# Kernel tuning notes

Hardware: AMD Instinct MI355X
Metric: run time of the kernel (lower is better)

The kernel has to match this reference:

```python
import jax, jax.numpy as jnp
import numpy as np

B, T, SD, AD, H, K, HID = 256, 128, 8, 2, 3, 4, 256


def setup_inputs() -> dict:
    key = jax.random.key(0)
    ks = jax.random.split(key, 12)
    inp = {
        "state": jax.random.normal(ks[0], (B, T, SD), dtype=jnp.float32),
        "action": jax.random.normal(ks[1], (B, T, AD), dtype=jnp.float32),
        # Linear(4, 4*H, bias=False): weight (4*H, 4)
        "Wk": jax.random.normal(ks[2], (4 * H, K), dtype=jnp.float32) * 0.1,
        "Wq": jax.random.normal(ks[3], (4 * H, SD + AD), dtype=jnp.float32) * 0.1,
        "Wv": jax.random.normal(ks[4], (4 * H, K), dtype=jnp.float32) * 0.1,
        # MLP: in_dim = 4*H + SD + AD -> HID -> HID -> 1
        "W1": jax.random.normal(ks[5], (HID, 4 * H + SD + AD), dtype=jnp.float32) * 0.05,
        "b1": jnp.zeros((HID,), dtype=jnp.float32),
        "W2": jax.random.normal(ks[6], (HID, HID), dtype=jnp.float32) * 0.05,
        "b2": jnp.zeros((HID,), dtype=jnp.float32),
        "Wout": jax.random.uniform(ks[7], (1, HID), minval=-0.003, maxval=0.003, dtype=jnp.float32),
        "bout": jax.random.uniform(ks[8], (1,), minval=-0.003, maxval=0.003, dtype=jnp.float32),
    }
    return inp


def reference(state, action, Wk, Wq, Wv, W1, b1, W2, b2, Wout, bout):
    q_state = jnp.concatenate([state, action], axis=-1)  # (b, t, sd+ad)
    s = state[:, :, :4]                                   # (b, t, 4)
    b, t, k = s.shape
    h = Wk.shape[0] // k
    # rel_full[b, i, j] = s[b, j] - s[b, i]  (matches torch view/transpose)
    rel_full = s[:, None, :, :] - s[:, :, None, :]        # (b, t, t, 4)
    # drop diagonal (self-pairs): idx[i] = all j != i, in order
    j = jnp.arange(t - 1)
    idx = j[None, :] + (j[None, :] >= jnp.arange(t)[:, None])  # (t, t-1)
    rel = jnp.take_along_axis(rel_full, idx[None, :, :, None], axis=2)  # (b, t, t-1, 4)
    # QKV projections (tiny head dim k=4)
    q = (q_state @ Wq.T).reshape(b, t, h, k)              # (b, t, h, 4)
    keys = (rel @ Wk.T).reshape(b, t, t - 1, h, k)        # (b, t, t-1, h, 4)
    vals = (rel @ Wv.T).reshape(b, t, t - 1, h, k)
    scores = jnp.einsum('bthk,btjhk->bthj', q, keys) / jnp.sqrt(jnp.float32(k))
    w = jax.nn.softmax(scores, axis=-1)                   # over the t-1 neighbors
    x = jnp.einsum('bthj,btjhk->bthk', w, vals).reshape(b, t, h * k)
    x = jnp.concatenate([x, q_state], axis=-1)            # (b, t, h*4 + sd+ad)
    x = jax.nn.relu(x @ W1.T + b1)
    x = jax.nn.relu(x @ W2.T + b2)
    return x @ Wout.T + bout                              # (b, t, 1)
```

## Files before the change

### kernel.cpp

```cpp
#include <hip/hip_runtime.h>
#include <math.h>

#define Bp 256
#define Tp 128
#define SDp 8
#define ADp 2
#define Hp 3
#define Kp 4
#define HIDp 256
#define QDp (SDp + ADp)
#define X1Dp (Hp * Kp + QDp)
#define QKLD 20
#define LOG2E 1.4426950408889634f

typedef short bf16x8 __attribute__((ext_vector_type(8)));
typedef float f32x4  __attribute__((ext_vector_type(4)));

__device__ __forceinline__ unsigned short f2bf(float f) {
    unsigned u = __float_as_uint(f);
    unsigned r = (u + 0x7FFFu + ((u >> 16) & 1u)) >> 16;
    return (unsigned short)r;
}

__device__ __forceinline__ unsigned h1_byte(int row, int colbytes) {
    return (((unsigned)row << 9) + (unsigned)colbytes) ^ ((unsigned)(row & 7) << 4);
}
__device__ __forceinline__ unsigned x1_byte(int row, int colbytes) {
    return ((unsigned)row << 6) + ((unsigned)colbytes ^ (((unsigned)row & 6u) << 3));
}

__global__ __launch_bounds__(256) void prep_kernel(
    const float* __restrict__ W1, const float* __restrict__ W2,
    unsigned short* __restrict__ W1b, unsigned short* __restrict__ W2b)
{
    const int bid = blockIdx.x;
    const int tid = threadIdx.x;
    if (bid < 64) {
        const int i = bid * 1024 + tid * 4;
        const float4 v = *(const float4*)(W2 + i);
        ushort4 o;
        o.x = f2bf(v.x); o.y = f2bf(v.y); o.z = f2bf(v.z); o.w = f2bf(v.w);
        *(ushort4*)(W2b + i) = o;
    } else {
        const int i = (bid - 64) * 256 + tid;
        const int r = i >> 5, c = i & 31;
        W1b[i] = (c < X1Dp) ? f2bf(W1[r * X1Dp + c]) : (unsigned short)0;
    }
}

__global__ __launch_bounds__(256, 4) void main_kernel(
    const float* __restrict__ state, const float* __restrict__ action,
    const float* __restrict__ Wk, const float* __restrict__ Wq,
    const float* __restrict__ Wv,
    const unsigned short* __restrict__ W1b, const unsigned short* __restrict__ W2b,
    const float* __restrict__ b1, const float* __restrict__ b2,
    const float* __restrict__ Wout, const float* __restrict__ bout,
    float* __restrict__ out)
{
    const int bid   = blockIdx.x;
    const int batch = bid >> 2;
    const int t0    = (bid & 3) * 32;
    const int tid   = threadIdx.x;
    const int lane  = tid & 63;
    const int wave  = tid >> 6;
    const int quad  = lane >> 4;
    const int l16   = lane & 15;
    const int t_loc = tid >> 3;
    const int jo    = tid & 7;
    const int t     = t0 + t_loc;

    __shared__ float4 s4[Tp];
    __shared__ float  wq[Hp * Kp * QDp];
    __shared__ float  wk[Hp * Kp * Kp];
    __shared__ float  wv[Hp * Kp * Kp];
    __shared__ float  qk[32 * QKLD];
    __shared__ __align__(16) unsigned short X1s[32 * 32];
    __shared__ __align__(16) unsigned short h1s[32 * 256];
    __shared__ float partial[4][32];

    if (tid < Tp)
        s4[tid] = ((const float4*)(state + (size_t)batch * Tp * SDp))[tid * 2];
    if (tid >= Tp && tid < Tp + Hp * Kp * QDp)
        wq[tid - Tp] = Wq[tid - Tp];
    if (tid < Hp * Kp * Kp) { wk[tid] = Wk[tid]; wv[tid] = Wv[tid]; }
    __syncthreads();

    if (tid < 32) {
        const int tt = t0 + tid;
        const float* srow = state + ((size_t)batch * Tp + tt) * SDp;
        float qs[QDp];
        {
            const float4 v0 = *(const float4*)srow;
            const float4 v1 = *(const float4*)(srow + 4);
            qs[0]=v0.x; qs[1]=v0.y; qs[2]=v0.z; qs[3]=v0.w;
            qs[4]=v1.x; qs[5]=v1.y; qs[6]=v1.z; qs[7]=v1.w;
            const float* arow = action + ((size_t)batch * Tp + tt) * ADp;
            qs[8] = arow[0]; qs[9] = arow[1];
        }
        float q[Hp * Kp];
        #pragma unroll
        for (int r = 0; r < Hp * Kp; ++r) {
            float a = 0.f;
            #pragma unroll
            for (int d = 0; d < QDp; ++d) a += qs[d] * wq[r * QDp + d];
            q[r] = a;
        }
        float* qrow = &qk[tid * QKLD];
        const float4 st = s4[tt];
        #pragma unroll
        for (int h = 0; h < Hp; ++h) {
            float p[4];
            #pragma unroll
            for (int c = 0; c < Kp; ++c) {
                float a = 0.f;
                #pragma unroll
                for (int k = 0; k < Kp; ++k) a += q[h * Kp + k] * wk[(h * Kp + k) * Kp + c];
                p[c] = 0.5f * LOG2E * a;
                qrow[h * 4 + c] = p[c];
            }
            qrow[12 + h] = st.x * p[0] + st.y * p[1] + st.z * p[2] + st.w * p[3];
        }
        #pragma unroll
        for (int i = 0; i < 5; ++i) {
            const unsigned u = (unsigned)f2bf(qs[2*i]) | ((unsigned)f2bf(qs[2*i+1]) << 16);
            qrow[15 + i] = __uint_as_float(u);
        }
    }
    __syncthreads();

    float rq[20];
    #pragma unroll
    for (int i = 0; i < 5; ++i)
        *(float4*)&rq[i * 4] = *(const float4*)&qk[t_loc * QKLD + i * 4];

    float l[Hp] = {0.f, 0.f, 0.f};
    float ac[Hp][4] = {};
    #pragma unroll
    for (int i = 0; i < 16; ++i) {
        const int j = (jo << 4) | ((i + jo) & 15);
        const float4 sj = s4[j];
        #pragma unroll
        for (int h = 0; h < Hp; ++h) {
            const float d = sj.x * rq[h*4] + sj.y * rq[h*4+1]
                          + sj.z * rq[h*4+2] + sj.w * rq[h*4+3] - rq[12 + h];
            const float e = (j == t) ? 0.f : __builtin_amdgcn_exp2f(d);
            l[h] += e;
            ac[h][0] += e * sj.x; ac[h][1] += e * sj.y;
            ac[h][2] += e * sj.z; ac[h][3] += e * sj.w;
        }
    }
    #pragma unroll
    for (int off = 1; off < 8; off <<= 1) {
        #pragma unroll
        for (int h = 0; h < Hp; ++h) {
            l[h] += __shfl_xor(l[h], off);
            #pragma unroll
            for (int c = 0; c < Kp; ++c) ac[h][c] += __shfl_xor(ac[h][c], off);
        }
    }

    if (jo == 0) {
        const float4 st = s4[t];
        unsigned short rowb[32] __attribute__((aligned(16)));
        #pragma unroll
        for (int h = 0; h < Hp; ++h) {
            const float inv = 1.f / l[h];
            const float rb0 = ac[h][0] * inv - st.x;
            const float rb1 = ac[h][1] * inv - st.y;
            const float rb2 = ac[h][2] * inv - st.z;
            const float rb3 = ac[h][3] * inv - st.w;
            #pragma unroll
            for (int k = 0; k < Kp; ++k) {
                const int r = h * Kp + k;
                rowb[r] = f2bf(rb0 * wv[r*4] + rb1 * wv[r*4+1] + rb2 * wv[r*4+2] + rb3 * wv[r*4+3]);
            }
        }
        #pragma unroll
        for (int i = 0; i < 5; ++i) {
            const unsigned u = __float_as_uint(rq[15 + i]);
            rowb[12 + 2*i] = (unsigned short)(u & 0xffffu);
            rowb[13 + 2*i] = (unsigned short)(u >> 16);
        }
        #pragma unroll
        for (int i = X1Dp; i < 32; ++i) rowb[i] = 0;

        const uint4* srcv = (const uint4*)rowb;
        #pragma unroll
        for (int i = 0; i < 4; ++i)
            *(uint4*)((char*)X1s + x1_byte(t_loc, i * 16)) = srcv[i];
    }
    __syncthreads();

    {
        const int rt  = wave & 1;
        const int chh = wave >> 1;
        const bf16x8 afr = *(const bf16x8*)((const char*)X1s +
                             x1_byte(rt * 16 + l16, quad * 16));
        #pragma unroll
        for (int n8 = 0; n8 < 8; ++n8) {
            const int col = chh * 128 + n8 * 16 + l16;
            const bf16x8 bfr = *(const bf16x8*)&W1b[col * 32 + quad * 8];
            f32x4 acc = {0.f, 0.f, 0.f, 0.f};
            acc = __builtin_amdgcn_mfma_f32_16x16x32_bf16(afr, bfr, acc, 0, 0, 0);
            const float bb = b1[col];
            #pragma unroll
            for (int r = 0; r < 4; ++r) {
                const int row = rt * 16 + quad * 4 + r;
                *(unsigned short*)((char*)h1s + h1_byte(row, col * 2)) =
                    f2bf(fmaxf(acc[r] + bb, 0.f));
            }
        }
    }
    __syncthreads();

    bf16x8 A[2][8];
    #pragma unroll
    for (int rt2 = 0; rt2 < 2; ++rt2)
        #pragma unroll
        for (int ks = 0; ks < 8; ++ks)
            A[rt2][ks] = *(const bf16x8*)((const char*)h1s +
                           h1_byte(rt2 * 16 + l16, ks * 64 + quad * 16));

    float rsum[2][4] = {};
    #pragma unroll
    for (int i = 0; i < 4; ++i) {
        const int col = (wave * 4 + i) * 16 + l16;
        const unsigned short* wr = W2b + (size_t)col * HIDp + quad * 8;
        bf16x8 Bf[8];
        #pragma unroll
        for (int ks = 0; ks < 8; ++ks)
            Bf[ks] = *(const bf16x8*)(wr + ks * 32);
        const float bb = b2[col];
        const float wo = Wout[col];
        #pragma unroll
        for (int rt2 = 0; rt2 < 2; ++rt2) {
            f32x4 acc = {0.f, 0.f, 0.f, 0.f};
            #pragma unroll
            for (int ks = 0; ks < 8; ++ks)
                acc = __builtin_amdgcn_mfma_f32_16x16x32_bf16(A[rt2][ks], Bf[ks], acc, 0, 0, 0);
            #pragma unroll
            for (int r = 0; r < 4; ++r)
                rsum[rt2][r] += fmaxf(acc[r] + bb, 0.f) * wo;
        }
    }

    #pragma unroll
    for (int off = 1; off < 16; off <<= 1)
        #pragma unroll
        for (int rt2 = 0; rt2 < 2; ++rt2)
            #pragma unroll
            for (int r = 0; r < 4; ++r)
                rsum[rt2][r] += __shfl_xor(rsum[rt2][r], off);

    if (l16 == 0) {
        #pragma unroll
        for (int rt2 = 0; rt2 < 2; ++rt2)
            #pragma unroll
            for (int r = 0; r < 4; ++r)
                partial[wave][rt2 * 16 + quad * 4 + r] = rsum[rt2][r];
    }
    __syncthreads();

    if (tid < 32) {
        out[(size_t)batch * Tp + t0 + tid] =
            partial[0][tid] + partial[1][tid] + partial[2][tid]
          + partial[3][tid] + bout[0];
    }
}

extern "C" void kernel_launch(void* const* d_in, const int* in_sizes, int n_in,
                              void* d_out, int out_size, void* d_ws, size_t ws_size,
                              hipStream_t stream) {
    const float* state  = (const float*)d_in[0];
    const float* action = (const float*)d_in[1];
    const float* Wk     = (const float*)d_in[2];
    const float* Wq     = (const float*)d_in[3];
    const float* Wv     = (const float*)d_in[4];
    const float* W1     = (const float*)d_in[5];
    const float* b1     = (const float*)d_in[6];
    const float* W2     = (const float*)d_in[7];
    const float* b2     = (const float*)d_in[8];
    const float* Wout   = (const float*)d_in[9];
    const float* bout   = (const float*)d_in[10];
    float* out = (float*)d_out;

    char* ws = (char*)d_ws;
    unsigned short* W1b = (unsigned short*)(ws);
    unsigned short* W2b = (unsigned short*)(ws + 16384);

    prep_kernel<<<96, 256, 0, stream>>>(W1, W2, W1b, W2b);
    main_kernel<<<4 * Bp, 256, 0, stream>>>(state, action, Wk, Wq, Wv,
                                            W1b, W2b, b1, b2, Wout, bout, out);
}
```

Baseline: 99.36 us.

## Double threads per block and split attention and MLP work across 8 waves

Raises the block size from 256 to 512 threads. The attention loop now uses 16 threads per query with 8 neighbors each, and the MLP column tiles are spread over 8 waves. The q projection now reads Wq/Wk straight from global memory and runs in parallel with the state staging, which removes one barrier. The diagonal is no longer masked in the inner loop; its exp term is subtracted after the reduction. This adds shuffle steps, raises per-block register and LDS pressure, and the after-the-fact subtraction is less precise.

```diff
diff --git a/kernel.cpp b/kernel.cpp
--- a/kernel.cpp
+++ b/kernel.cpp
@@ -10,7 +10,7 @@
 #define HIDp 256
 #define QDp (SDp + ADp)
 #define X1Dp (Hp * Kp + QDp)
-#define QKLD 20
+#define QKLD 17
 #define LOG2E 1.4426950408889634f
 
 typedef short bf16x8 __attribute__((ext_vector_type(8)));
@@ -48,7 +48,7 @@
     }
 }
 
-__global__ __launch_bounds__(256, 4) void main_kernel(
+__global__ __launch_bounds__(512, 6) void main_kernel(
     const float* __restrict__ state, const float* __restrict__ action,
     const float* __restrict__ Wk, const float* __restrict__ Wq,
     const float* __restrict__ Wv,
@@ -65,31 +65,25 @@
     const int wave  = tid >> 6;
     const int quad  = lane >> 4;
     const int l16   = lane & 15;
-    const int t_loc = tid >> 3;
-    const int jo    = tid & 7;
+    const int t_loc = tid >> 4;
+    const int jo    = tid & 15;
     const int t     = t0 + t_loc;
 
     __shared__ float4 s4[Tp];
-    __shared__ float  wq[Hp * Kp * QDp];
-    __shared__ float  wk[Hp * Kp * Kp];
     __shared__ float  wv[Hp * Kp * Kp];
     __shared__ float  qk[32 * QKLD];
     __shared__ __align__(16) unsigned short X1s[32 * 32];
     __shared__ __align__(16) unsigned short h1s[32 * 256];
-    __shared__ float partial[4][32];
-
-    if (tid < Tp)
+    __shared__ float partial[8][32];
+
+    if (tid < Tp) {
         s4[tid] = ((const float4*)(state + (size_t)batch * Tp * SDp))[tid * 2];
-    if (tid >= Tp && tid < Tp + Hp * Kp * QDp)
-        wq[tid - Tp] = Wq[tid - Tp];
-    if (tid < Hp * Kp * Kp) { wk[tid] = Wk[tid]; wv[tid] = Wv[tid]; }
-    __syncthreads();
-
-    if (tid < 32) {
-        const int tt = t0 + tid;
-        const float* srow = state + ((size_t)batch * Tp + tt) * SDp;
+    } else if (tid < 160) {
+        const int ta = tid - 128;
+        const int tt = t0 + ta;
         float qs[QDp];
         {
+            const float* srow = state + ((size_t)batch * Tp + tt) * SDp;
             const float4 v0 = *(const float4*)srow;
             const float4 v1 = *(const float4*)(srow + 4);
             qs[0]=v0.x; qs[1]=v0.y; qs[2]=v0.z; qs[3]=v0.w;
@@ -102,55 +96,52 @@
         for (int r = 0; r < Hp * Kp; ++r) {
             float a = 0.f;
             #pragma unroll
-            for (int d = 0; d < QDp; ++d) a += qs[d] * wq[r * QDp + d];
+            for (int d = 0; d < QDp; ++d) a += qs[d] * Wq[r * QDp + d];
             q[r] = a;
         }
-        float* qrow = &qk[tid * QKLD];
-        const float4 st = s4[tt];
-        #pragma unroll
-        for (int h = 0; h < Hp; ++h) {
-            float p[4];
+        float* qrow = &qk[ta * QKLD];
+        #pragma unroll
+        for (int h = 0; h < Hp; ++h)
             #pragma unroll
             for (int c = 0; c < Kp; ++c) {
                 float a = 0.f;
                 #pragma unroll
-                for (int k = 0; k < Kp; ++k) a += q[h * Kp + k] * wk[(h * Kp + k) * Kp + c];
-                p[c] = 0.5f * LOG2E * a;
-                qrow[h * 4 + c] = p[c];
+                for (int k = 0; k < Kp; ++k) a += q[h * Kp + k] * Wk[(h * Kp + k) * Kp + c];
+                qrow[h * 4 + c] = 0.5f * LOG2E * a;
             }
-            qrow[12 + h] = st.x * p[0] + st.y * p[1] + st.z * p[2] + st.w * p[3];
-        }
         #pragma unroll
         for (int i = 0; i < 5; ++i) {
             const unsigned u = (unsigned)f2bf(qs[2*i]) | ((unsigned)f2bf(qs[2*i+1]) << 16);
-            qrow[15 + i] = __uint_as_float(u);
-        }
-    }
-    __syncthreads();
-
-    float rq[20];
-    #pragma unroll
-    for (int i = 0; i < 5; ++i)
+            qrow[12 + i] = __uint_as_float(u);
+        }
+    } else if (tid < 160 + Hp * Kp * Kp) {
+        wv[tid - 160] = Wv[tid - 160];
+    }
+    __syncthreads();
+
+    float rq[12];
+    #pragma unroll
+    for (int i = 0; i < 3; ++i)
         *(float4*)&rq[i * 4] = *(const float4*)&qk[t_loc * QKLD + i * 4];
 
     float l[Hp] = {0.f, 0.f, 0.f};
     float ac[Hp][4] = {};
     #pragma unroll
-    for (int i = 0; i < 16; ++i) {
-        const int j = (jo << 4) | ((i + jo) & 15);
+    for (int i = 0; i < 8; ++i) {
+        const int j = (jo << 3) | ((i + jo) & 7);
         const float4 sj = s4[j];
         #pragma unroll
         for (int h = 0; h < Hp; ++h) {
             const float d = sj.x * rq[h*4] + sj.y * rq[h*4+1]
-                          + sj.z * rq[h*4+2] + sj.w * rq[h*4+3] - rq[12 + h];
-            const float e = (j == t) ? 0.f : __builtin_amdgcn_exp2f(d);
+                          + sj.z * rq[h*4+2] + sj.w * rq[h*4+3];
+            const float e = __builtin_amdgcn_exp2f(d);
             l[h] += e;
             ac[h][0] += e * sj.x; ac[h][1] += e * sj.y;
             ac[h][2] += e * sj.z; ac[h][3] += e * sj.w;
         }
     }
     #pragma unroll
-    for (int off = 1; off < 8; off <<= 1) {
+    for (int off = 1; off < 16; off <<= 1) {
         #pragma unroll
         for (int h = 0; h < Hp; ++h) {
             l[h] += __shfl_xor(l[h], off);
@@ -164,11 +155,14 @@
         unsigned short rowb[32] __attribute__((aligned(16)));
         #pragma unroll
         for (int h = 0; h < Hp; ++h) {
-            const float inv = 1.f / l[h];
-            const float rb0 = ac[h][0] * inv - st.x;
-            const float rb1 = ac[h][1] * inv - st.y;
-            const float rb2 = ac[h][2] * inv - st.z;
-            const float rb3 = ac[h][3] * inv - st.w;
+            const float dtt = st.x * rq[h*4] + st.y * rq[h*4+1]
+                            + st.z * rq[h*4+2] + st.w * rq[h*4+3];
+            const float ett = __builtin_amdgcn_exp2f(dtt);
+            const float inv = 1.f / (l[h] - ett);
+            const float rb0 = (ac[h][0] - ett * st.x) * inv - st.x;
+            const float rb1 = (ac[h][1] - ett * st.y) * inv - st.y;
+            const float rb2 = (ac[h][2] - ett * st.z) * inv - st.z;
+            const float rb3 = (ac[h][3] - ett * st.w) * inv - st.w;
             #pragma unroll
             for (int k = 0; k < Kp; ++k) {
                 const int r = h * Kp + k;
@@ -177,7 +171,7 @@
         }
         #pragma unroll
         for (int i = 0; i < 5; ++i) {
-            const unsigned u = __float_as_uint(rq[15 + i]);
+            const unsigned u = __float_as_uint(qk[t_loc * QKLD + 12 + i]);
             rowb[12 + 2*i] = (unsigned short)(u & 0xffffu);
             rowb[13 + 2*i] = (unsigned short)(u >> 16);
         }
@@ -197,8 +191,8 @@
         const bf16x8 afr = *(const bf16x8*)((const char*)X1s +
                              x1_byte(rt * 16 + l16, quad * 16));
         #pragma unroll
-        for (int n8 = 0; n8 < 8; ++n8) {
-            const int col = chh * 128 + n8 * 16 + l16;
+        for (int n = 0; n < 4; ++n) {
+            const int col = chh * 64 + n * 16 + l16;
             const bf16x8 bfr = *(const bf16x8*)&W1b[col * 32 + quad * 8];
             f32x4 acc = {0.f, 0.f, 0.f, 0.f};
             acc = __builtin_amdgcn_mfma_f32_16x16x32_bf16(afr, bfr, acc, 0, 0, 0);
@@ -213,18 +207,10 @@
     }
     __syncthreads();
 
-    bf16x8 A[2][8];
-    #pragma unroll
-    for (int rt2 = 0; rt2 < 2; ++rt2)
-        #pragma unroll
-        for (int ks = 0; ks < 8; ++ks)
-            A[rt2][ks] = *(const bf16x8*)((const char*)h1s +
-                           h1_byte(rt2 * 16 + l16, ks * 64 + quad * 16));
-
     float rsum[2][4] = {};
     #pragma unroll
-    for (int i = 0; i < 4; ++i) {
-        const int col = (wave * 4 + i) * 16 + l16;
+    for (int i = 0; i < 2; ++i) {
+        const int col = wave * 32 + i * 16 + l16;
         const unsigned short* wr = W2b + (size_t)col * HIDp + quad * 8;
         bf16x8 Bf[8];
         #pragma unroll
@@ -233,38 +219,44 @@
         const float bb = b2[col];
         const float wo = Wout[col];
         #pragma unroll
-        for (int rt2 = 0; rt2 < 2; ++rt2) {
+        for (int rt = 0; rt < 2; ++rt) {
+            bf16x8 A8[8];
+            #pragma unroll
+            for (int ks = 0; ks < 8; ++ks)
+                A8[ks] = *(const bf16x8*)((const char*)h1s +
+                           h1_byte(rt * 16 + l16, ks * 64 + quad * 16));
             f32x4 acc = {0.f, 0.f, 0.f, 0.f};
             #pragma unroll
             for (int ks = 0; ks < 8; ++ks)
-                acc = __builtin_amdgcn_mfma_f32_16x16x32_bf16(A[rt2][ks], Bf[ks], acc, 0, 0, 0);
+                acc = __builtin_amdgcn_mfma_f32_16x16x32_bf16(A8[ks], Bf[ks], acc, 0, 0, 0);
             #pragma unroll
             for (int r = 0; r < 4; ++r)
-                rsum[rt2][r] += fmaxf(acc[r] + bb, 0.f) * wo;
+                rsum[rt][r] += fmaxf(acc[r] + bb, 0.f) * wo;
         }
     }
 
     #pragma unroll
     for (int off = 1; off < 16; off <<= 1)
         #pragma unroll
-        for (int rt2 = 0; rt2 < 2; ++rt2)
+        for (int rt = 0; rt < 2; ++rt)
             #pragma unroll
             for (int r = 0; r < 4; ++r)
-                rsum[rt2][r] += __shfl_xor(rsum[rt2][r], off);
+                rsum[rt][r] += __shfl_xor(rsum[rt][r], off);
 
     if (l16 == 0) {
         #pragma unroll
-        for (int rt2 = 0; rt2 < 2; ++rt2)
+        for (int rt = 0; rt < 2; ++rt)
             #pragma unroll
             for (int r = 0; r < 4; ++r)
-                partial[wave][rt2 * 16 + quad * 4 + r] = rsum[rt2][r];
+                partial[wave][rt * 16 + quad * 4 + r] = rsum[rt][r];
     }
     __syncthreads();
 
     if (tid < 32) {
-        out[(size_t)batch * Tp + t0 + tid] =
-            partial[0][tid] + partial[1][tid] + partial[2][tid]
-          + partial[3][tid] + bout[0];
+        float o = bout[0];
+        #pragma unroll
+        for (int w = 0; w < 8; ++w) o += partial[w][tid];
+        out[(size_t)batch * Tp + t0 + tid] = o;
     }
 }
 
@@ -289,6 +281,6 @@
     unsigned short* W2b = (unsigned short*)(ws + 16384);
 
     prep_kernel<<<96, 256, 0, stream>>>(W1, W2, W1b, W2b);
-    main_kernel<<<4 * Bp, 256, 0, stream>>>(state, action, Wk, Wq, Wv,
+    main_kernel<<<4 * Bp, 512, 0, stream>>>(state, action, Wk, Wq, Wv,
                                             W1b, W2b, b1, b2, Wout, bout, out);
 }
```

Measured after the change: 102.6 us. 1.03x slower.
